# Kernel tuning notes

Measured on AMD Instinct MI355X. Metric: run time of the kernel, lower is better.

## Reference

```python
import jax, jax.numpy as jnp
import numpy as np
import math

B, S, D, H = 2, 2048, 1024, 16
HS = D // H  # head_size = 64


def setup_inputs() -> dict:
    key = jax.random.key(0)
    ks = jax.random.split(key, 5)
    scale = 0.02
    return {
        "q": jax.random.normal(ks[0], (B, S, D), dtype=jnp.float32),
        "Wq": jax.random.normal(ks[1], (D, D), dtype=jnp.float32) * scale,
        "bq": jnp.zeros((D,), dtype=jnp.float32),
        "Wk": jax.random.normal(ks[2], (D, D), dtype=jnp.float32) * scale,
        "bk": jnp.zeros((D,), dtype=jnp.float32),
        "Wv": jax.random.normal(ks[3], (D, D), dtype=jnp.float32) * scale,
        "bv": jnp.zeros((D,), dtype=jnp.float32),
        "Wo": jax.random.normal(ks[4], (D, D), dtype=jnp.float32) * scale,
        "bo": jnp.zeros((D,), dtype=jnp.float32),
    }


def reference(q, Wq, bq, Wk, bk, Wv, bv, Wo, bo) -> jnp.ndarray:
    # self-attention: k = v = q (source defaults), is_causal=True, dropout=0 (eval)
    b, s, d = q.shape
    qh = (q @ Wq + bq).reshape(b, s, H, HS).transpose(0, 2, 1, 3)  # [B,H,S,HS]
    kh = (q @ Wk + bk).reshape(b, s, H, HS).transpose(0, 2, 1, 3)
    vh = (q @ Wv + bv).reshape(b, s, H, HS).transpose(0, 2, 1, 3)
    scores = jnp.einsum("bhqd,bhkd->bhqk", qh, kh) / math.sqrt(HS)  # [B,H,S,S]
    causal = jnp.triu(jnp.ones((s, s), dtype=bool), k=1)
    scores = jnp.where(causal, -jnp.inf, scores)
    attn = jax.nn.softmax(scores, axis=-1)
    out = jnp.einsum("bhqk,bhkd->bhqd", attn, vh)  # [B,H,S,HS]
    out = out.transpose(0, 2, 1, 3).reshape(b, s, d)
    return out @ Wo + bo
```

## Files before the change

### kernel.cpp

```cpp
#include <hip/hip_runtime.h>
#include <hip/hip_bf16.h>

typedef unsigned short u16;
typedef __attribute__((ext_vector_type(8))) __bf16 bf16x8;
typedef __attribute__((ext_vector_type(4))) float f32x4;

#define S_LEN 2048
#define DMODEL 1024
#define NHEAD 16
#define HSZ 64

__device__ __forceinline__ u16 f2bf(float f) {
  union { __hip_bfloat16 b; u16 u; } c;
  c.b = __float2bfloat16(f);
  return c.u;
}

__device__ __forceinline__ float bf2f(u16 u) {
  union { unsigned int i; float f; } c;
  c.i = ((unsigned int)u) << 16;
  return c.f;
}

__device__ __forceinline__ float fexp2(float x) {
#if __has_builtin(__builtin_amdgcn_exp2f)
  return __builtin_amdgcn_exp2f(x);
#else
  return exp2f(x);
#endif
}

__device__ __forceinline__ unsigned int cvtpk(float lo, float hi) {
  unsigned int r;
  asm("v_cvt_pk_bf16_f32 %0, %1, %2" : "=v"(r) : "v"(lo), "v"(hi));
  return r;
}

__device__ __forceinline__ void gload_lds16(const void* g, void* l) {
  __builtin_amdgcn_global_load_lds(
      (const __attribute__((address_space(1))) void*)g,
      (__attribute__((address_space(3))) void*)l, 16, 0, 0);
}

__device__ __forceinline__ f32x4 mfma16(bf16x8 a, bf16x8 b, f32x4 c) {
  return __builtin_amdgcn_mfma_f32_16x16x32_bf16(a, b, c, 0, 0, 0);
}

__global__ __launch_bounds__(256) void convert_f2b_kernel(const float* __restrict__ in,
                                                          u16* __restrict__ out) {
  int i = (blockIdx.x * 256 + threadIdx.x) * 4;
  float4 v = *(const float4*)(in + i);
  ushort4 o;
  o.x = f2bf(v.x); o.y = f2bf(v.y); o.z = f2bf(v.z); o.w = f2bf(v.w);
  *(ushort4*)(out + i) = o;
}

__global__ __launch_bounds__(256) void transpose_w_kernel(
    const float* __restrict__ W0, const float* __restrict__ W1,
    const float* __restrict__ W2, const float* __restrict__ W3,
    u16* __restrict__ T0, u16* __restrict__ T1,
    u16* __restrict__ T2, u16* __restrict__ T3) {
  int z = blockIdx.z;
  const float* W = (z == 0) ? W0 : ((z == 1) ? W1 : ((z == 2) ? W2 : W3));
  u16* T = (z == 0) ? T0 : ((z == 1) ? T1 : ((z == 2) ? T2 : T3));
  __shared__ float tile[64][65];
  int t = threadIdx.x;
  int k0 = blockIdx.y * 64, n0 = blockIdx.x * 64;
#pragma unroll
  for (int j = 0; j < 4; ++j) {
    int idx = j * 256 + t;
    int row = idx >> 4, c4 = idx & 15;
    float4 v = *(const float4*)(W + (size_t)(k0 + row) * DMODEL + n0 + c4 * 4);
    tile[row][c4 * 4 + 0] = v.x; tile[row][c4 * 4 + 1] = v.y;
    tile[row][c4 * 4 + 2] = v.z; tile[row][c4 * 4 + 3] = v.w;
  }
  __syncthreads();
#pragma unroll
  for (int j = 0; j < 4; ++j) {
    int idx = j * 256 + t;
    int orow = idx >> 4, c4 = idx & 15;
    ushort4 o;
    o.x = f2bf(tile[c4 * 4 + 0][orow]);
    o.y = f2bf(tile[c4 * 4 + 1][orow]);
    o.z = f2bf(tile[c4 * 4 + 2][orow]);
    o.w = f2bf(tile[c4 * 4 + 3][orow]);
    *(ushort4*)(T + (size_t)(n0 + orow) * DMODEL + k0 + c4 * 4) = o;
  }
}

__global__ __launch_bounds__(256) void transpose_v_kernel(const u16* __restrict__ Vh,
                                                          u16* __restrict__ Vt) {
  int bh = blockIdx.y;
  int s0 = blockIdx.x * 64;
  __shared__ __align__(16) u16 tile[64][72];
  int t = threadIdx.x;
#pragma unroll
  for (int j = 0; j < 4; ++j) {
    int idx = j * 256 + t;
    int row = idx >> 4, c4 = idx & 15;
    *(ushort4*)&tile[row][c4 * 4] =
        *(const ushort4*)(Vh + ((size_t)bh * S_LEN + s0 + row) * HSZ + c4 * 4);
  }
  __syncthreads();
#pragma unroll
  for (int j = 0; j < 4; ++j) {
    int idx = j * 256 + t;
    int orow = idx >> 4, c4 = idx & 15;
    ushort4 o;
    o.x = tile[c4 * 4 + 0][orow];
    o.y = tile[c4 * 4 + 1][orow];
    o.z = tile[c4 * 4 + 2][orow];
    o.w = tile[c4 * 4 + 3][orow];
    *(ushort4*)(Vt + ((size_t)bh * HSZ + orow) * S_LEN + s0 + c4 * 4) = o;
  }
}

template <int WM>
__device__ __forceinline__ void gemm_core(const u16* __restrict__ A,
                                          const u16* __restrict__ Bt,
                                          u16* ldsbuf, f32x4 (&acc)[WM][4],
                                          int m0, int n0) {
  const int t = threadIdx.x;
  const int wave = t >> 6, lane = t & 63;
  const int l15 = lane & 15, l4 = lane >> 4;
  const int wr = wave >> 1, wc = wave & 1;
  u16* Asm = ldsbuf;
  u16* Bsm = ldsbuf + WM * 1024;
  for (int kt = 0; kt < DMODEL / 32; ++kt) {
    int kb = kt * 32;
#pragma unroll
    for (int j = 0; j < WM / 2; ++j) {
      int ci = j * 256 + t;
      int row = ci >> 2, kc = ci & 3;
      gload_lds16(A + (size_t)(m0 + row) * DMODEL + kb + kc * 8,
                  Asm + (j * 256 + wave * 64) * 8);
    }
#pragma unroll
    for (int j = 0; j < 2; ++j) {
      int ci = j * 256 + t;
      int row = ci >> 2, kc = ci & 3;
      gload_lds16(Bt + (size_t)(n0 + row) * DMODEL + kb + kc * 8,
                  Bsm + (j * 256 + wave * 64) * 8);
    }
    __syncthreads();
    bf16x8 af[WM], bfr[4];
#pragma unroll
    for (int m = 0; m < WM; ++m)
      af[m] = *(const bf16x8*)(Asm + ((wr * (WM * 16) + m * 16 + l15) * 32 + l4 * 8));
#pragma unroll
    for (int n = 0; n < 4; ++n)
      bfr[n] = *(const bf16x8*)(Bsm + ((wc * 64 + n * 16 + l15) * 32 + l4 * 8));
#pragma unroll
    for (int m = 0; m < WM; ++m)
#pragma unroll
      for (int n = 0; n < 4; ++n)
        acc[m][n] = mfma16(af[m], bfr[n], acc[m][n]);
    __syncthreads();
  }
}

__global__ __launch_bounds__(256) void gemm_qkv_kernel(
    const u16* __restrict__ A, const u16* __restrict__ B0, const u16* __restrict__ B1,
    const u16* __restrict__ B2, const float* __restrict__ bias0,
    const float* __restrict__ bias1, const float* __restrict__ bias2,
    u16* __restrict__ d0, u16* __restrict__ d1, u16* __restrict__ d2) {
  __shared__ __align__(16) u16 lds[8192];
  int z = blockIdx.z;
  const u16* Bt = (z == 0) ? B0 : ((z == 1) ? B1 : B2);
  const float* bias = (z == 0) ? bias0 : ((z == 1) ? bias1 : bias2);
  u16* dst = (z == 0) ? d0 : ((z == 1) ? d1 : d2);
  const float sc = (z == 0) ? 0.18033688011112042f : 1.0f;
  int m0 = blockIdx.y * 128, n0 = blockIdx.x * 128;
  f32x4 acc[4][4] = {};
  gemm_core<4>(A, Bt, lds, acc, m0, n0);
  const int t = threadIdx.x;
  const int wave = t >> 6, lane = t & 63, l15 = lane & 15, l4 = lane >> 4;
  const int wr = wave >> 1, wc = wave & 1;
#pragma unroll
  for (int n = 0; n < 4; ++n) {
    int colg = n0 + wc * 64 + n * 16 + l15;
    float bn = bias[colg];
    int h = colg >> 6, hs = colg & 63;
#pragma unroll
    for (int m = 0; m < 4; ++m) {
#pragma unroll
      for (int i = 0; i < 4; ++i) {
        int rowg = m0 + wr * 64 + m * 16 + 4 * l4 + i;
        int b = rowg >> 11, s = rowg & 2047;
        dst[(size_t)(b * NHEAD + h) * S_LEN * HSZ + (size_t)s * HSZ + hs] =
            f2bf((acc[m][n][i] + bn) * sc);
      }
    }
  }
}

__global__ __launch_bounds__(256) void gemm_out_kernel(const u16* __restrict__ A,
                                                       const u16* __restrict__ Bt,
                                                       const float* __restrict__ bias,
                                                       float* __restrict__ out) {
  __shared__ __align__(16) u16 lds[6144];
  int m0 = blockIdx.y * 64, n0 = blockIdx.x * 128;
  f32x4 acc[2][4] = {};
  gemm_core<2>(A, Bt, lds, acc, m0, n0);
  const int t = threadIdx.x;
  const int wave = t >> 6, lane = t & 63, l15 = lane & 15, l4 = lane >> 4;
  const int wr = wave >> 1, wc = wave & 1;
#pragma unroll
  for (int n = 0; n < 4; ++n) {
    int colg = n0 + wc * 64 + n * 16 + l15;
    float bn = bias[colg];
#pragma unroll
    for (int m = 0; m < 2; ++m) {
#pragma unroll
      for (int i = 0; i < 4; ++i) {
        int rowg = m0 + wr * 32 + m * 16 + 4 * l4 + i;
        out[(size_t)rowg * DMODEL + colg] = acc[m][n][i] + bn;
      }
    }
  }
}

__global__ __launch_bounds__(256, 2) void attn_kernel(const u16* __restrict__ Qh,
                                                      const u16* __restrict__ Kh,
                                                      const u16* __restrict__ Vt,
                                                      u16* __restrict__ Ob) {
  __shared__ __align__(16) u16 Ksm[64][72];
  __shared__ __align__(16) u16 Vsm[64][72];
  __shared__ __align__(16) u16 Pl[4][32][72];
  const int tixd = threadIdx.x;
  const int wave = tixd >> 6, lane = tixd & 63;
  const int l15 = lane & 15, l4 = lane >> 4;
  const int id = blockIdx.x;
  const int bh = (id & 7) * 4 + ((id >> 3) & 3);
  const int pk = id >> 5;
  const u16* Qb = Qh + (size_t)bh * S_LEN * HSZ;
  const u16* Kb = Kh + (size_t)bh * S_LEN * HSZ;
  const u16* Vb = Vt + (size_t)bh * HSZ * S_LEN;
  const int shbase = l4 * 20;
  u16 (*P)[72] = Pl[wave];
  const int b = bh >> 4, h = bh & 15;
  const int sr = tixd >> 2;
  const int scb = (tixd & 3) * 16;

#pragma unroll 1
  for (int ph = 0; ph < 2; ++ph) {
    const int pp = ph ? (15 - pk) : pk;
    const int q0 = pp * 128 + wave * 32;
    const int nt = 2 * pp + 2;

    bf16x8 qf[2][2];
#pragma unroll
    for (int m = 0; m < 2; ++m)
#pragma unroll
      for (int kc = 0; kc < 2; ++kc)
        qf[m][kc] = *(const bf16x8*)(Qb + (size_t)(q0 + m * 16 + l15) * HSZ + kc * 32 + l4 * 8);

    f32x4 oacc[2][4] = {};
    float mrun[2] = {-1e30f, -1e30f};
    float lrun[2] = {0.f, 0.f};

    uint4 ka0 = *(const uint4*)(Kb + (size_t)sr * HSZ + scb);
    uint4 ka1 = *(const uint4*)(Kb + (size_t)sr * HSZ + scb + 8);
    uint4 va0 = *(const uint4*)(Vb + (size_t)sr * S_LEN + scb);
    uint4 va1 = *(const uint4*)(Vb + (size_t)sr * S_LEN + scb + 8);

#pragma unroll 1
    for (int t = 0; t < nt; ++t) {
      __syncthreads();
      *(uint4*)&Ksm[sr][scb]     = ka0;
      *(uint4*)&Ksm[sr][scb + 8] = ka1;
      *(uint4*)&Vsm[sr][scb]     = va0;
      *(uint4*)&Vsm[sr][scb + 8] = va1;
      __syncthreads();
      if (t + 1 < nt) {
        const int kvn = (t + 1) * 64;
        ka0 = *(const uint4*)(Kb + (size_t)(kvn + sr) * HSZ + scb);
        ka1 = *(const uint4*)(Kb + (size_t)(kvn + sr) * HSZ + scb + 8);
        va0 = *(const uint4*)(Vb + (size_t)sr * S_LEN + kvn + scb);
        va1 = *(const uint4*)(Vb + (size_t)sr * S_LEN + kvn + scb + 8);
      }
      const int kv0 = t * 64;

      bf16x8 kf[4][2];
#pragma unroll
      for (int n = 0; n < 4; ++n)
#pragma unroll
        for (int kc = 0; kc < 2; ++kc)
          kf[n][kc] = *(const bf16x8*)&Ksm[n * 16 + l15][kc * 32 + l4 * 8];

      f32x4 sacc[2][4] = {};
#pragma unroll
      for (int m = 0; m < 2; ++m)
#pragma unroll
        for (int n = 0; n < 4; ++n) {
          sacc[m][n] = mfma16(kf[n][0], qf[m][0], sacc[m][n]);
          sacc[m][n] = mfma16(kf[n][1], qf[m][1], sacc[m][n]);
        }

      bf16x8 vf[2][4];
#pragma unroll
      for (int kb = 0; kb < 2; ++kb)
#pragma unroll
        for (int n = 0; n < 4; ++n)
          vf[kb][n] = *(const bf16x8*)&Vsm[n * 16 + l15][kb * 32 + l4 * 8];

      if (kv0 + 63 > q0) {
#pragma unroll
        for (int m = 0; m < 2; ++m)
#pragma unroll
          for (int n = 0; n < 4; ++n)
#pragma unroll
            for (int i = 0; i < 4; ++i)
              if (kv0 + n * 16 + 4 * l4 + i > q0 + m * 16 + l15) sacc[m][n][i] = -1e30f;
      }

#pragma unroll
      for (int m = 0; m < 2; ++m) {
        float a0 = fmaxf(fmaxf(sacc[m][0][0], sacc[m][0][1]),
                         fmaxf(sacc[m][0][2], sacc[m][0][3]));
        float a1 = fmaxf(fmaxf(sacc[m][1][0], sacc[m][1][1]),
                         fmaxf(sacc[m][1][2], sacc[m][1][3]));
        float a2 = fmaxf(fmaxf(sacc[m][2][0], sacc[m][2][1]),
                         fmaxf(sacc[m][2][2], sacc[m][2][3]));
        float a3 = fmaxf(fmaxf(sacc[m][3][0], sacc[m][3][1]),
                         fmaxf(sacc[m][3][2], sacc[m][3][3]));
        float tm = fmaxf(fmaxf(a0, a1), fmaxf(a2, a3));
        tm = fmaxf(tm, __shfl_xor(tm, 16));
        tm = fmaxf(tm, __shfl_xor(tm, 32));
        float mnew = fmaxf(mrun[m], tm);
        float corr = fexp2(mrun[m] - mnew);
        mrun[m] = mnew;
        float rs = 0.f;
#pragma unroll
        for (int n = 0; n < 4; ++n)
#pragma unroll
          for (int i = 0; i < 4; ++i) {
            float pv = fexp2(sacc[m][n][i] - mnew);
            sacc[m][n][i] = pv;
            rs += pv;
          }
        rs += __shfl_xor(rs, 16);
        rs += __shfl_xor(rs, 32);
        lrun[m] = lrun[m] * corr + rs;
        float cc0 = __shfl(corr, shbase + 0);
        float cc1 = __shfl(corr, shbase + 1);
        float cc2 = __shfl(corr, shbase + 2);
        float cc3 = __shfl(corr, shbase + 3);
#pragma unroll
        for (int n = 0; n < 4; ++n) {
          oacc[m][n][0] *= cc0; oacc[m][n][1] *= cc1;
          oacc[m][n][2] *= cc2; oacc[m][n][3] *= cc3;
        }
#pragma unroll
        for (int n = 0; n < 4; ++n) {
          uint2 pkk;
          pkk.x = cvtpk(sacc[m][n][0], sacc[m][n][1]);
          pkk.y = cvtpk(sacc[m][n][2], sacc[m][n][3]);
          *(uint2*)&P[m * 16 + l15][n * 16 + 4 * l4] = pkk;
        }
      }

#pragma unroll
      for (int kb = 0; kb < 2; ++kb) {
        bf16x8 pf0 = *(const bf16x8*)&P[l15][kb * 32 + l4 * 8];
        bf16x8 pf1 = *(const bf16x8*)&P[16 + l15][kb * 32 + l4 * 8];
#pragma unroll
        for (int n = 0; n < 4; ++n) {
          oacc[0][n] = mfma16(pf0, vf[kb][n], oacc[0][n]);
          oacc[1][n] = mfma16(pf1, vf[kb][n], oacc[1][n]);
        }
      }
    }

#pragma unroll
    for (int m = 0; m < 2; ++m) {
      float invm = 1.0f / lrun[m];
#pragma unroll
      for (int i = 0; i < 4; ++i) {
        float iv = __shfl(invm, shbase + i);
        int srow = q0 + m * 16 + 4 * l4 + i;
#pragma unroll
        for (int n = 0; n < 4; ++n) {
          int d = h * HSZ + n * 16 + l15;
          Ob[((size_t)b * S_LEN + srow) * DMODEL + d] = f2bf(oacc[m][n][i] * iv);
        }
      }
    }
  }
}

extern "C" void kernel_launch(void* const* d_in, const int* in_sizes, int n_in,
                              void* d_out, int out_size, void* d_ws, size_t ws_size,
                              hipStream_t stream) {
  const float* q  = (const float*)d_in[0];
  const float* Wq = (const float*)d_in[1];
  const float* bq = (const float*)d_in[2];
  const float* Wk = (const float*)d_in[3];
  const float* bk = (const float*)d_in[4];
  const float* Wv = (const float*)d_in[5];
  const float* bv = (const float*)d_in[6];
  const float* Wo = (const float*)d_in[7];
  const float* bo = (const float*)d_in[8];

  char* ws = (char*)d_ws;
  const size_t MB = 1024 * 1024;
  u16* Xb  = (u16*)(ws + 0);
  u16* WqT = (u16*)(ws + 8 * MB);
  u16* WkT = (u16*)(ws + 10 * MB);
  u16* WvT = (u16*)(ws + 12 * MB);
  u16* WoT = (u16*)(ws + 14 * MB);
  u16* Qh  = (u16*)(ws + 16 * MB);
  u16* Kh  = (u16*)(ws + 24 * MB);
  u16* Vh  = (u16*)(ws + 32 * MB);
  u16* Vt  = (u16*)(ws + 40 * MB);
  u16* Ob  = (u16*)(ws + 48 * MB);

  convert_f2b_kernel<<<4096, 256, 0, stream>>>(q, Xb);
  transpose_w_kernel<<<dim3(16, 16, 4), 256, 0, stream>>>(Wq, Wk, Wv, Wo,
                                                          WqT, WkT, WvT, WoT);
  gemm_qkv_kernel<<<dim3(8, 32, 3), 256, 0, stream>>>(Xb, WqT, WkT, WvT,
                                                      bq, bk, bv, Qh, Kh, Vh);
  transpose_v_kernel<<<dim3(32, 32), 256, 0, stream>>>(Vh, Vt);
  attn_kernel<<<256, 256, 0, stream>>>(Qh, Kh, Vt, Ob);
  gemm_out_kernel<<<dim3(8, 64), 256, 0, stream>>>(Ob, WoT, bo, (float*)d_out);
}
```

Measured before the change: 118.5 us.

## Split attention block into eight waves of sixteen query rows each

The attention kernel now launches 512 threads per block, and each of the eight waves owns 16 query rows instead of each of four waves owning 32. This halves per-wave accumulator and score registers and doubles the waves available to hide latency. Each thread now stages a single 16-byte K and V chunk per tile. The cost is that every wave reloads the full K and V fragments from shared memory for only 16 rows, which doubles LDS read traffic per MFMA, and barrier synchronisation now spans more waves.

```diff
diff --git a/kernel.cpp b/kernel.cpp
--- a/kernel.cpp
+++ b/kernel.cpp
@@ -220,13 +220,13 @@
   }
 }
 
-__global__ __launch_bounds__(256, 2) void attn_kernel(const u16* __restrict__ Qh,
+__global__ __launch_bounds__(512, 2) void attn_kernel(const u16* __restrict__ Qh,
                                                       const u16* __restrict__ Kh,
                                                       const u16* __restrict__ Vt,
                                                       u16* __restrict__ Ob) {
   __shared__ __align__(16) u16 Ksm[64][72];
   __shared__ __align__(16) u16 Vsm[64][72];
-  __shared__ __align__(16) u16 Pl[4][32][72];
+  __shared__ __align__(16) u16 Pl[8][16][72];
   const int tixd = threadIdx.x;
   const int wave = tixd >> 6, lane = tixd & 63;
   const int l15 = lane & 15, l4 = lane >> 4;
@@ -239,45 +239,37 @@
   const int shbase = l4 * 20;
   u16 (*P)[72] = Pl[wave];
   const int b = bh >> 4, h = bh & 15;
-  const int sr = tixd >> 2;
-  const int scb = (tixd & 3) * 16;
+  const int sr = tixd >> 3;
+  const int sc = (tixd & 7) * 8;
 
 #pragma unroll 1
   for (int ph = 0; ph < 2; ++ph) {
     const int pp = ph ? (15 - pk) : pk;
-    const int q0 = pp * 128 + wave * 32;
+    const int q0 = pp * 128 + wave * 16;
     const int nt = 2 * pp + 2;
 
-    bf16x8 qf[2][2];
-#pragma unroll
-    for (int m = 0; m < 2; ++m)
-#pragma unroll
-      for (int kc = 0; kc < 2; ++kc)
-        qf[m][kc] = *(const bf16x8*)(Qb + (size_t)(q0 + m * 16 + l15) * HSZ + kc * 32 + l4 * 8);
-
-    f32x4 oacc[2][4] = {};
-    float mrun[2] = {-1e30f, -1e30f};
-    float lrun[2] = {0.f, 0.f};
-
-    uint4 ka0 = *(const uint4*)(Kb + (size_t)sr * HSZ + scb);
-    uint4 ka1 = *(const uint4*)(Kb + (size_t)sr * HSZ + scb + 8);
-    uint4 va0 = *(const uint4*)(Vb + (size_t)sr * S_LEN + scb);
-    uint4 va1 = *(const uint4*)(Vb + (size_t)sr * S_LEN + scb + 8);
+    bf16x8 qf[2];
+#pragma unroll
+    for (int kc = 0; kc < 2; ++kc)
+      qf[kc] = *(const bf16x8*)(Qb + (size_t)(q0 + l15) * HSZ + kc * 32 + l4 * 8);
+
+    f32x4 oacc[4] = {};
+    float mrun = -1e30f;
+    float lrun = 0.f;
+
+    uint4 ka = *(const uint4*)(Kb + (size_t)sr * HSZ + sc);
+    uint4 va = *(const uint4*)(Vb + (size_t)sr * S_LEN + sc);
 
 #pragma unroll 1
     for (int t = 0; t < nt; ++t) {
       __syncthreads();
-      *(uint4*)&Ksm[sr][scb]     = ka0;
-      *(uint4*)&Ksm[sr][scb + 8] = ka1;
-      *(uint4*)&Vsm[sr][scb]     = va0;
-      *(uint4*)&Vsm[sr][scb + 8] = va1;
+      *(uint4*)&Ksm[sr][sc] = ka;
+      *(uint4*)&Vsm[sr][sc] = va;
       __syncthreads();
       if (t + 1 < nt) {
         const int kvn = (t + 1) * 64;
-        ka0 = *(const uint4*)(Kb + (size_t)(kvn + sr) * HSZ + scb);
-        ka1 = *(const uint4*)(Kb + (size_t)(kvn + sr) * HSZ + scb + 8);
-        va0 = *(const uint4*)(Vb + (size_t)sr * S_LEN + kvn + scb);
-        va1 = *(const uint4*)(Vb + (size_t)sr * S_LEN + kvn + scb + 8);
+        ka = *(const uint4*)(Kb + (size_t)(kvn + sr) * HSZ + sc);
+        va = *(const uint4*)(Vb + (size_t)sr * S_LEN + kvn + sc);
       }
       const int kv0 = t * 64;
 
@@ -288,14 +280,12 @@
         for (int kc = 0; kc < 2; ++kc)
           kf[n][kc] = *(const bf16x8*)&Ksm[n * 16 + l15][kc * 32 + l4 * 8];
 
-      f32x4 sacc[2][4] = {};
-#pragma unroll
-      for (int m = 0; m < 2; ++m)
-#pragma unroll
-        for (int n = 0; n < 4; ++n) {
-          sacc[m][n] = mfma16(kf[n][0], qf[m][0], sacc[m][n]);
-          sacc[m][n] = mfma16(kf[n][1], qf[m][1], sacc[m][n]);
-        }
+      f32x4 sacc[4] = {};
+#pragma unroll
+      for (int n = 0; n < 4; ++n) {
+        sacc[n] = mfma16(kf[n][0], qf[0], sacc[n]);
+        sacc[n] = mfma16(kf[n][1], qf[1], sacc[n]);
+      }
 
       bf16x8 vf[2][4];
 #pragma unroll
@@ -306,83 +296,76 @@
 
       if (kv0 + 63 > q0) {
 #pragma unroll
-        for (int m = 0; m < 2; ++m)
-#pragma unroll
-          for (int n = 0; n < 4; ++n)
-#pragma unroll
-            for (int i = 0; i < 4; ++i)
-              if (kv0 + n * 16 + 4 * l4 + i > q0 + m * 16 + l15) sacc[m][n][i] = -1e30f;
-      }
-
-#pragma unroll
-      for (int m = 0; m < 2; ++m) {
-        float a0 = fmaxf(fmaxf(sacc[m][0][0], sacc[m][0][1]),
-                         fmaxf(sacc[m][0][2], sacc[m][0][3]));
-        float a1 = fmaxf(fmaxf(sacc[m][1][0], sacc[m][1][1]),
-                         fmaxf(sacc[m][1][2], sacc[m][1][3]));
-        float a2 = fmaxf(fmaxf(sacc[m][2][0], sacc[m][2][1]),
-                         fmaxf(sacc[m][2][2], sacc[m][2][3]));
-        float a3 = fmaxf(fmaxf(sacc[m][3][0], sacc[m][3][1]),
-                         fmaxf(sacc[m][3][2], sacc[m][3][3]));
+        for (int n = 0; n < 4; ++n)
+#pragma unroll
+          for (int i = 0; i < 4; ++i)
+            if (kv0 + n * 16 + 4 * l4 + i > q0 + l15) sacc[n][i] = -1e30f;
+      }
+
+      {
+        float a0 = fmaxf(fmaxf(sacc[0][0], sacc[0][1]),
+                         fmaxf(sacc[0][2], sacc[0][3]));
+        float a1 = fmaxf(fmaxf(sacc[1][0], sacc[1][1]),
+                         fmaxf(sacc[1][2], sacc[1][3]));
+        float a2 = fmaxf(fmaxf(sacc[2][0], sacc[2][1]),
+                         fmaxf(sacc[2][2], sacc[2][3]));
+        float a3 = fmaxf(fmaxf(sacc[3][0], sacc[3][1]),
+                         fmaxf(sacc[3][2], sacc[3][3]));
         float tm = fmaxf(fmaxf(a0, a1), fmaxf(a2, a3));
         tm = fmaxf(tm, __shfl_xor(tm, 16));
         tm = fmaxf(tm, __shfl_xor(tm, 32));
-        float mnew = fmaxf(mrun[m], tm);
-        float corr = fexp2(mrun[m] - mnew);
-        mrun[m] = mnew;
+        float mnew = fmaxf(mrun, tm);
+        float corr = fexp2(mrun - mnew);
+        mrun = mnew;
         float rs = 0.f;
 #pragma unroll
         for (int n = 0; n < 4; ++n)
 #pragma unroll
           for (int i = 0; i < 4; ++i) {
-            float pv = fexp2(sacc[m][n][i] - mnew);
-            sacc[m][n][i] = pv;
+            float pv = fexp2(sacc[n][i] - mnew);
+            sacc[n][i] = pv;
             rs += pv;
           }
         rs += __shfl_xor(rs, 16);
         rs += __shfl_xor(rs, 32);
-        lrun[m] = lrun[m] * corr + rs;
+        lrun = lrun * corr + rs;
         float cc0 = __shfl(corr, shbase + 0);
         float cc1 = __shfl(corr, shbase + 1);
         float cc2 = __shfl(corr, shbase + 2);
         float cc3 = __shfl(corr, shbase + 3);
 #pragma unroll
         for (int n = 0; n < 4; ++n) {
-          oacc[m][n][0] *= cc0; oacc[m][n][1] *= cc1;
-          oacc[m][n][2] *= cc2; oacc[m][n][3] *= cc3;
+          oacc[n][0] *= cc0; oacc[n][1] *= cc1;
+          oacc[n][2] *= cc2; oacc[n][3] *= cc3;
         }
 #pragma unroll
         for (int n = 0; n < 4; ++n) {
           uint2 pkk;
-          pkk.x = cvtpk(sacc[m][n][0], sacc[m][n][1]);
-          pkk.y = cvtpk(sacc[m][n][2], sacc[m][n][3]);
-          *(uint2*)&P[m * 16 + l15][n * 16 + 4 * l4] = pkk;
+          pkk.x = cvtpk(sacc[n][0], sacc[n][1]);
+          pkk.y = cvtpk(sacc[n][2], sacc[n][3]);
+          *(uint2*)&P[l15][n * 16 + 4 * l4] = pkk;
         }
       }
 
 #pragma unroll
       for (int kb = 0; kb < 2; ++kb) {
-        bf16x8 pf0 = *(const bf16x8*)&P[l15][kb * 32 + l4 * 8];
-        bf16x8 pf1 = *(const bf16x8*)&P[16 + l15][kb * 32 + l4 * 8];
-#pragma unroll
-        for (int n = 0; n < 4; ++n) {
-          oacc[0][n] = mfma16(pf0, vf[kb][n], oacc[0][n]);
-          oacc[1][n] = mfma16(pf1, vf[kb][n], oacc[1][n]);
-        }
-      }
-    }
-
-#pragma unroll
-    for (int m = 0; m < 2; ++m) {
-      float invm = 1.0f / lrun[m];
+        bf16x8 pf = *(const bf16x8*)&P[l15][kb * 32 + l4 * 8];
+#pragma unroll
+        for (int n = 0; n < 4; ++n)
+          oacc[n] = mfma16(pf, vf[kb][n], oacc[n]);
+      }
+    }
+
+    {
+      float invm = 1.0f / lrun;
 #pragma unroll
       for (int i = 0; i < 4; ++i) {
         float iv = __shfl(invm, shbase + i);
-        int srow = q0 + m * 16 + 4 * l4 + i;
+        int srow = q0 + 4 * l4 + i;
 #pragma unroll
         for (int n = 0; n < 4; ++n) {
           int d = h * HSZ + n * 16 + l15;
-          Ob[((size_t)b * S_LEN + srow) * DMODEL + d] = f2bf(oacc[m][n][i] * iv);
+          Ob[((size_t)b * S_LEN + srow) * DMODEL + d] = f2bf(oacc[n][i] * iv);
         }
       }
     }
@@ -421,6 +404,6 @@
   gemm_qkv_kernel<<<dim3(8, 32, 3), 256, 0, stream>>>(Xb, WqT, WkT, WvT,
                                                       bq, bk, bv, Qh, Kh, Vh);
   transpose_v_kernel<<<dim3(32, 32), 256, 0, stream>>>(Vh, Vt);
-  attn_kernel<<<256, 256, 0, stream>>>(Qh, Kh, Vt, Ob);
+  attn_kernel<<<256, 512, 0, stream>>>(Qh, Kh, Vt, Ob);
   gemm_out_kernel<<<dim3(8, 64), 256, 0, stream>>>(Ob, WoT, bo, (float*)d_out);
 }
```

Measured after the change: 115.9 us. -2.2%, faster.
